# Kernel optimization log

Measured on AMD Instinct MI355X. Metric: run time of the kernel, lower is better.

## Reference

```python
import jax, jax.numpy as jnp
import numpy as np

N, E, D_EDGE, C, H, W, HID = 10000, 160000, 64, 16, 8, 8, 128


def setup_inputs() -> dict:
    key = jax.random.key(0)
    ks = jax.random.split(key, 7)
    x = jax.random.normal(ks[0], (N, C, H, W), jnp.float32)
    edge_attr = jax.random.normal(ks[1], (E, D_EDGE), jnp.float32)
    edge_index = jax.random.randint(ks[2], (2, E), 0, N, dtype=jnp.int64)
    W1 = jax.random.normal(ks[3], (D_EDGE, HID), jnp.float32) * 0.1
    b1 = jnp.zeros((HID,), jnp.float32)
    W2 = jax.random.normal(ks[4], (HID, 1), jnp.float32) * 0.1
    b2 = jnp.zeros((1,), jnp.float32)
    Wn = jax.random.normal(ks[5], (C, 3 * C), jnp.float32) * 0.1
    bn = jnp.zeros((C,), jnp.float32)
    return dict(x=x, edge_attr=edge_attr, W1=W1, b1=b1, W2=W2, b2=b2,
                Wn=Wn, bn=bn, edge_index=edge_index)


def _masked_scatter_softmax(logits, seg, mask, n):
    # softmax over edges grouped by seg, restricted to mask==True edges.
    # Masked edges get -inf logits -> exp 0 -> zero weight (same math as
    # boolean-indexing the edge subset in the torch original).
    neg = jnp.where(mask[:, None], logits, -jnp.inf)          # [E, 1]
    m = jax.ops.segment_max(neg, seg, num_segments=n)         # [N, 1]
    m = jnp.where(jnp.isfinite(m), m, 0.0)                    # empty segments
    e = jnp.exp(neg - m[seg])                                 # [E, 1], 0 where masked
    s = jax.ops.segment_sum(e, seg, num_segments=n)           # [N, 1]
    return e / jnp.maximum(s[seg], 1e-30)


def _flow(x, logits, row, col, mask, n):
    w = _masked_scatter_softmax(logits, row, mask, n)         # [E, 1]
    msg = x[col] * w[:, :, None, None]                        # [E, C, H, W]
    return jax.ops.segment_sum(msg, row, num_segments=n)      # [N, C, H, W]


def reference(x, edge_attr, W1, b1, W2, b2, Wn, bn, edge_index):
    row, col = edge_index[0], edge_index[1]
    # cls_net: MLP edge classifier producing per-edge logit [E, 1]
    h = jax.nn.relu(edge_attr @ W1 + b1)
    dec_edge_feats = h @ W2 + b2
    n = x.shape[0]
    flow_out = _flow(x, dec_edge_feats, row, col, row < col, n)
    flow_in = _flow(x, dec_edge_feats, row, col, row > col, n)
    flow = jnp.concatenate([x, flow_in, flow_out], axis=1)    # [N, 3C, H, W]
    # node_model: 1x1 conv over channels
    out = jnp.einsum('nchw,oc->nohw', flow, Wn) + bn[None, :, None, None]
    return out, dec_edge_feats
```

## Files before the change

### kernel.cpp

```cpp
#include <hip/hip_runtime.h>

#define N_NODES 10000
#define N_EDGES 160000
#define D_EDGE  64
#define C_CH    16
#define HW      64
#define HID     128
#define NODE_ELEMS 1024
#define NSEG    (2 * N_NODES)
#define CAP     64
#define MLPB    (N_EDGES / 64)
#define QUANTB  2500

typedef __attribute__((ext_vector_type(8))) short short8;
typedef __attribute__((ext_vector_type(4))) float f32x4;

__device__ __forceinline__ unsigned bf16_rne(float f) {
    unsigned u = __float_as_uint(f);
    return (u + 0x7FFFu + ((u >> 16) & 1u)) >> 16;
}
__device__ __forceinline__ short8 pack_bf16x8(float4 lo, float4 hi) {
    union { unsigned u[4]; short8 s; } r;
    r.u[0] = bf16_rne(lo.x) | (bf16_rne(lo.y) << 16);
    r.u[1] = bf16_rne(lo.z) | (bf16_rne(lo.w) << 16);
    r.u[2] = bf16_rne(hi.x) | (bf16_rne(hi.y) << 16);
    r.u[3] = bf16_rne(hi.z) | (bf16_rne(hi.w) << 16);
    return r.s;
}

__global__ __launch_bounds__(256) void k_prep(
    const float* __restrict__ W1, unsigned short* __restrict__ W1bfT,
    unsigned* __restrict__ zbase)
{
    if (blockIdx.x < 4) {
        int q  = blockIdx.x * 256 + threadIdx.x;
        int n  = q >> 3;
        int ko = (q & 7) * 8;
        #pragma unroll
        for (int i = 0; i < 8; ++i) {
            int k = ko + i;
            W1bfT[n * 64 + k] = (unsigned short)bf16_rne(W1[k * HID + n]);
        }
    } else {
        int idx = (blockIdx.x - 4) * 256 + threadIdx.x;
        for (int i = idx; i < NSEG; i += 64 * 256) zbase[i] = 0u;
    }
}

__device__ __forceinline__ unsigned pb4(float4 f, float inv) {
    int a = (int)rintf(f.x * inv) + 128;
    int b = (int)rintf(f.y * inv) + 128;
    int c = (int)rintf(f.z * inv) + 128;
    int d = (int)rintf(f.w * inv) + 128;
    a = min(255, max(0, a)); b = min(255, max(0, b));
    c = min(255, max(0, c)); d = min(255, max(0, d));
    return (unsigned)a | ((unsigned)b << 8) | ((unsigned)c << 16) | ((unsigned)d << 24);
}
__global__ __launch_bounds__(256) void k_mlpcast(
    const float* __restrict__ ea, const unsigned short* __restrict__ W1bfT,
    const float* __restrict__ b1, const float* __restrict__ W2,
    const float* __restrict__ b2,
    const int* __restrict__ row, const int* __restrict__ col,
    const float* __restrict__ x, unsigned char* __restrict__ xq,
    float* __restrict__ scale,
    float* __restrict__ dec,
    int* __restrict__ cursor, int2* __restrict__ bucket)
{
    const int tid = threadIdx.x;

    if (blockIdx.x >= MLPB) {
        const int wv = tid >> 6, ln = tid & 63;
        const int n  = (blockIdx.x - MLPB) * 4 + wv;
        const float4* xs = (const float4*)(x + (size_t)n * NODE_ELEMS) + ln * 4;
        float4 v0 = xs[0], v1 = xs[1], v2 = xs[2], v3 = xs[3];
        float m = fmaxf(fmaxf(fmaxf(fabsf(v0.x), fabsf(v0.y)),
                              fmaxf(fabsf(v0.z), fabsf(v0.w))),
                 fmaxf(fmaxf(fmaxf(fabsf(v1.x), fabsf(v1.y)),
                              fmaxf(fabsf(v1.z), fabsf(v1.w))),
                 fmaxf(fmaxf(fmaxf(fabsf(v2.x), fabsf(v2.y)),
                              fmaxf(fabsf(v2.z), fabsf(v2.w))),
                       fmaxf(fmaxf(fabsf(v3.x), fabsf(v3.y)),
                              fmaxf(fabsf(v3.z), fabsf(v3.w))))));
        #pragma unroll
        for (int off = 1; off < 64; off <<= 1)
            m = fmaxf(m, __shfl_xor(m, off));
        m = fmaxf(m, 1e-20f);
        float inv = 127.0f / m;
        uint4 o;
        o.x = pb4(v0, inv); o.y = pb4(v1, inv);
        o.z = pb4(v2, inv); o.w = pb4(v3, inv);
        ((uint4*)(xq + (size_t)n * NODE_ELEMS))[ln] = o;
        if (ln == 0) scale[n] = m * (1.0f / 127.0f);
        return;
    }

    __shared__ float s_w2[HID], s_b1[HID];
    __shared__ float s_logit[64];

    const int eb = blockIdx.x * 64;
    if (tid < HID) { s_w2[tid] = W2[tid]; s_b1[tid] = b1[tid]; }

    const int lane = tid & 63, w = tid >> 6;
    const int i15 = lane & 15, g = lane >> 4;
    const int m = w * 16 + i15;

    short8 bfrag[2][8];
    #pragma unroll
    for (int kt = 0; kt < 2; ++kt)
        #pragma unroll
        for (int t = 0; t < 8; ++t)
            bfrag[kt][t] = *(const short8*)&W1bfT[(t * 16 + i15) * 64 + kt * 32 + g * 8];

    short8 afrag[2];
    #pragma unroll
    for (int kt = 0; kt < 2; ++kt) {
        const float4* src = (const float4*)&ea[(size_t)(eb + m) * D_EDGE + kt * 32 + g * 8];
        afrag[kt] = pack_bf16x8(src[0], src[1]);
    }

    f32x4 acc[8];
    #pragma unroll
    for (int t = 0; t < 8; ++t) acc[t] = (f32x4){0.f, 0.f, 0.f, 0.f};
    #pragma unroll
    for (int kt = 0; kt < 2; ++kt)
        #pragma unroll
        for (int t = 0; t < 8; ++t)
            acc[t] = __builtin_amdgcn_mfma_f32_16x16x32_bf16(afrag[kt], bfrag[kt][t],
                                                             acc[t], 0, 0, 0);
    __syncthreads();

    float loc[4] = {0.f, 0.f, 0.f, 0.f};
    #pragma unroll
    for (int t = 0; t < 8; ++t) {
        float w2v = s_w2[t * 16 + i15];
        float bv  = s_b1[t * 16 + i15];
        #pragma unroll
        for (int r = 0; r < 4; ++r)
            loc[r] = fmaf(fmaxf(acc[t][r] + bv, 0.f), w2v, loc[r]);
    }
    #pragma unroll
    for (int r = 0; r < 4; ++r) {
        #pragma unroll
        for (int off = 1; off < 16; off <<= 1)
            loc[r] += __shfl_xor(loc[r], off);
    }
    if (i15 == 0) {
        #pragma unroll
        for (int r = 0; r < 4; ++r)
            s_logit[w * 16 + g * 4 + r] = loc[r];
    }
    __syncthreads();

    if (tid < 64) {
        int e = eb + tid;
        float logit = s_logit[tid] + b2[0];
        dec[e] = logit;
        int r = row[e], c = col[e];
        if (r != c) {
            float ex = expf(logit);
            int seg = 2 * r + ((r < c) ? 0 : 1);
            int pos = atomicAdd(&cursor[seg], 1);
            if (pos < CAP)
                bucket[((size_t)seg << 6) + pos] = make_int2(c, __float_as_int(ex));
        }
    }
}

__device__ __forceinline__ void acc8(float* A, uint2 v, float ws) {
    A[0] = fmaf(ws, (float)( v.x        & 255u), A[0]);
    A[1] = fmaf(ws, (float)((v.x >>  8) & 255u), A[1]);
    A[2] = fmaf(ws, (float)((v.x >> 16) & 255u), A[2]);
    A[3] = fmaf(ws, (float)( v.x >> 24        ), A[3]);
    A[4] = fmaf(ws, (float)( v.y        & 255u), A[4]);
    A[5] = fmaf(ws, (float)((v.y >>  8) & 255u), A[5]);
    A[6] = fmaf(ws, (float)((v.y >> 16) & 255u), A[6]);
    A[7] = fmaf(ws, (float)( v.y >> 24        ), A[7]);
}

__global__ __launch_bounds__(128) void k_gather(
    const float* __restrict__ x, const unsigned char* __restrict__ xq,
    const float* __restrict__ scale,
    const int* __restrict__ cursor, const int2* __restrict__ bucket,
    const float* __restrict__ Wn, const float* __restrict__ bn,
    float* __restrict__ out)
{
    const int n = blockIdx.x;
    const int t = threadIdx.x;

    __shared__ float sflow[2][NODE_ELEMS];
    __shared__ float sW[C_CH * 3 * C_CH];
    __shared__ float sbn[C_CH];
    __shared__ int2  s_ecw[2 * CAP];
    __shared__ float s_ex[2 * CAP];

    #pragma unroll
    for (int i = 0; i < 6; ++i) sW[i * 128 + t] = Wn[i * 128 + t];
    if (t < C_CH) sbn[t] = bn[t];

    const int c0  = min(cursor[2 * n],     CAP);
    const int c1  = min(cursor[2 * n + 1], CAP);
    const int tot = c0 + c1;
    if (t < tot) {
        int2 e = (t < c0) ? bucket[((size_t)(2 * n) << 6) + t]
                          : bucket[((size_t)(2 * n + 1) << 6) + t - c0];
        float ex = __int_as_float(e.y);
        s_ex[t] = ex;
        e.y = __float_as_int(ex * scale[e.x]);
        s_ecw[t] = e;
    }
    __syncthreads();

    float sum0 = 0.f, sum1 = 0.f;
    for (int i = 0; i < c0; ++i)   sum0 += s_ex[i];
    for (int i = c0; i < tot; ++i) sum1 += s_ex[i];

    float a[8] = {0,0,0,0,0,0,0,0};
    float b[8] = {0,0,0,0,0,0,0,0};
    float wsA = 0.f, wsB = 0.f;
    const uint2* xqt = (const uint2*)xq + t;

#define FMAJ(J) { float ws = __int_as_float(s_ecw[i + (J)].y);                \
                  if (i + (J) < c0) { acc8(a, v[J], ws); wsA += ws; }         \
                  else              { acc8(b, v[J], ws); wsB += ws; } }

    int i = 0;
    for (; i + 16 <= tot; i += 16) {
        uint2 v[16];
        #pragma unroll
        for (int j = 0; j < 16; ++j) v[j] = xqt[(size_t)s_ecw[i + j].x * 128];
        #pragma unroll
        for (int j = 0; j < 16; ++j) FMAJ(j)
    }
    for (; i + 8 <= tot; i += 8) {
        uint2 v[8];
        #pragma unroll
        for (int j = 0; j < 8; ++j) v[j] = xqt[(size_t)s_ecw[i + j].x * 128];
        #pragma unroll
        for (int j = 0; j < 8; ++j) FMAJ(j)
    }
    for (; i + 4 <= tot; i += 4) {
        uint2 v[4];
        #pragma unroll
        for (int j = 0; j < 4; ++j) v[j] = xqt[(size_t)s_ecw[i + j].x * 128];
        #pragma unroll
        for (int j = 0; j < 4; ++j) FMAJ(j)
    }
    for (; i < tot; ++i) {
        uint2 v[1];
        v[0] = xqt[(size_t)s_ecw[i].x * 128];
        FMAJ(0)
    }
#undef FMAJ

    const float r0 = 1.0f / fmaxf(sum0, 1e-30f);
    const float r1 = 1.0f / fmaxf(sum1, 1e-30f);
    const float o0 = 128.0f * wsA, o1 = 128.0f * wsB;
    float4 f;
    f.x = (a[0]-o0)*r0; f.y = (a[1]-o0)*r0; f.z = (a[2]-o0)*r0; f.w = (a[3]-o0)*r0;
    ((float4*)sflow[0])[t * 2] = f;
    f.x = (a[4]-o0)*r0; f.y = (a[5]-o0)*r0; f.z = (a[6]-o0)*r0; f.w = (a[7]-o0)*r0;
    ((float4*)sflow[0])[t * 2 + 1] = f;
    f.x = (b[0]-o1)*r1; f.y = (b[1]-o1)*r1; f.z = (b[2]-o1)*r1; f.w = (b[3]-o1)*r1;
    ((float4*)sflow[1])[t * 2] = f;
    f.x = (b[4]-o1)*r1; f.y = (b[5]-o1)*r1; f.z = (b[6]-o1)*r1; f.w = (b[7]-o1)*r1;
    ((float4*)sflow[1])[t * 2 + 1] = f;
    __syncthreads();

    const int hw = t & 63;
    const int ob = t >> 6;
    const float* xb0 = x + (size_t)n * NODE_ELEMS + hw;
    float vx[C_CH], vi[C_CH], vo[C_CH];
    #pragma unroll
    for (int c = 0; c < C_CH; ++c) {
        vx[c] = xb0[c * HW];
        vo[c] = sflow[0][c * HW + hw];
        vi[c] = sflow[1][c * HW + hw];
    }
    float* outb = out + (size_t)n * NODE_ELEMS;
    #pragma unroll
    for (int k = 0; k < 8; ++k) {
        int o = ob * 8 + k;
        float acc = sbn[o];
        const float* wr = &sW[o * 3 * C_CH];
        #pragma unroll
        for (int c = 0; c < C_CH; ++c) {
            acc = fmaf(vx[c], wr[c],            acc);
            acc = fmaf(vi[c], wr[C_CH + c],     acc);
            acc = fmaf(vo[c], wr[2 * C_CH + c], acc);
        }
        outb[o * HW + hw] = acc;
    }
}

extern "C" void kernel_launch(void* const* d_in, const int* in_sizes, int n_in,
                              void* d_out, int out_size, void* d_ws, size_t ws_size,
                              hipStream_t stream)
{
    const float* x         = (const float*)d_in[0];
    const float* edge_attr = (const float*)d_in[1];
    const float* W1        = (const float*)d_in[2];
    const float* b1        = (const float*)d_in[3];
    const float* W2        = (const float*)d_in[4];
    const float* b2        = (const float*)d_in[5];
    const float* Wn        = (const float*)d_in[6];
    const float* bn        = (const float*)d_in[7];
    const int*   eidx      = (const int*)d_in[8];
    const int*   row       = eidx;
    const int*   col       = eidx + N_EDGES;

    float* out = (float*)d_out;
    float* dec = out + (size_t)N_NODES * NODE_ELEMS;

    unsigned char* xq     = (unsigned char*)d_ws;
    float*         scale  = (float*)(xq + (size_t)N_NODES * NODE_ELEMS);
    int2*          bucket = (int2*)(scale + N_NODES);
    int*           cursor = (int*)(bucket + (size_t)NSEG * CAP);
    unsigned short* W1bfT = (unsigned short*)(cursor + NSEG);

    k_prep<<<68, 256, 0, stream>>>(W1, W1bfT, (unsigned*)cursor);
    k_mlpcast<<<MLPB + QUANTB, 256, 0, stream>>>(edge_attr, W1bfT, b1, W2, b2,
                                                 row, col, x, xq, scale,
                                                 dec, cursor, bucket);
    k_gather<<<N_NODES, 128, 0, stream>>>(x, xq, scale, cursor,
                                          bucket, Wn, bn, out);
}
```

Baseline: 86.31 us.

## Use bf16 MFMA for node 1x1 conv and hoist bucket atomics early

The per-node 1x1 channel conv in the gather kernel is rewritten as a bf16 MFMA 16x16x32 GEMM. x and both flows are staged transposed in padded bf16 shared memory, and Wn is pre-transposed and converted to bf16 in the prep kernel. In the MLP kernel, the row/col loads and bucket-slot atomics are moved before the MFMA work so their latency overlaps with compute. This cuts FP32 FMA work and shared-memory traffic but adds bf16 rounding error to the output.

```diff
diff --git a/kernel.cpp b/kernel.cpp
--- a/kernel.cpp
+++ b/kernel.cpp
@@ -11,6 +11,7 @@
 #define CAP     64
 #define MLPB    (N_EDGES / 64)
 #define QUANTB  2500
+#define XPITCH  72
 
 typedef __attribute__((ext_vector_type(8))) short short8;
 typedef __attribute__((ext_vector_type(4))) float f32x4;
@@ -29,11 +30,13 @@
 }
 
 __global__ __launch_bounds__(256) void k_prep(
-    const float* __restrict__ W1, unsigned short* __restrict__ W1bfT,
+    const float* __restrict__ W1, const float* __restrict__ Wn,
+    unsigned short* __restrict__ W1bfT, unsigned short* __restrict__ WnTb,
     unsigned* __restrict__ zbase)
 {
+    int tid = threadIdx.x;
     if (blockIdx.x < 4) {
-        int q  = blockIdx.x * 256 + threadIdx.x;
+        int q  = blockIdx.x * 256 + tid;
         int n  = q >> 3;
         int ko = (q & 7) * 8;
         #pragma unroll
@@ -41,8 +44,17 @@
             int k = ko + i;
             W1bfT[n * 64 + k] = (unsigned short)bf16_rne(W1[k * HID + n]);
         }
+    } else if (blockIdx.x == 4) {
+        int q = tid * 4;
+        int o = q >> 6, k0 = q & 63;
+        #pragma unroll
+        for (int i = 0; i < 4; ++i) {
+            int k = k0 + i;
+            WnTb[o * 64 + k] =
+                (k < 48) ? (unsigned short)bf16_rne(Wn[o * 48 + k]) : 0;
+        }
     } else {
-        int idx = (blockIdx.x - 4) * 256 + threadIdx.x;
+        int idx = (blockIdx.x - 5) * 256 + tid;
         for (int i = idx; i < NSEG; i += 64 * 256) zbase[i] = 0u;
     }
 }
@@ -98,6 +110,17 @@
     __shared__ float s_logit[64];
 
     const int eb = blockIdx.x * 64;
+
+    int e_c = 0, pos = -1, seg = 0;
+    if (tid < 64) {
+        int e = eb + tid;
+        int r = row[e]; e_c = col[e];
+        if (r != e_c) {
+            seg = 2 * r + ((r < e_c) ? 0 : 1);
+            pos = atomicAdd(&cursor[seg], 1);
+        }
+    }
+
     if (tid < HID) { s_w2[tid] = W2[tid]; s_b1[tid] = b1[tid]; }
 
     const int lane = tid & 63, w = tid >> 6;
@@ -152,16 +175,11 @@
     __syncthreads();
 
     if (tid < 64) {
-        int e = eb + tid;
         float logit = s_logit[tid] + b2[0];
-        dec[e] = logit;
-        int r = row[e], c = col[e];
-        if (r != c) {
+        dec[eb + tid] = logit;
+        if (pos >= 0 && pos < CAP) {
             float ex = expf(logit);
-            int seg = 2 * r + ((r < c) ? 0 : 1);
-            int pos = atomicAdd(&cursor[seg], 1);
-            if (pos < CAP)
-                bucket[((size_t)seg << 6) + pos] = make_int2(c, __float_as_int(ex));
+            bucket[((size_t)seg << 6) + pos] = make_int2(e_c, __float_as_int(ex));
         }
     }
 }
@@ -181,21 +199,20 @@
     const float* __restrict__ x, const unsigned char* __restrict__ xq,
     const float* __restrict__ scale,
     const int* __restrict__ cursor, const int2* __restrict__ bucket,
-    const float* __restrict__ Wn, const float* __restrict__ bn,
+    const unsigned short* __restrict__ WnTb, const float* __restrict__ bn,
     float* __restrict__ out)
 {
     const int n = blockIdx.x;
     const int t = threadIdx.x;
 
-    __shared__ float sflow[2][NODE_ELEMS];
-    __shared__ float sW[C_CH * 3 * C_CH];
-    __shared__ float sbn[C_CH];
+    __shared__ __align__(16) unsigned short sxf[64 * XPITCH];
     __shared__ int2  s_ecw[2 * CAP];
     __shared__ float s_ex[2 * CAP];
 
-    #pragma unroll
-    for (int i = 0; i < 6; ++i) sW[i * 128 + t] = Wn[i * 128 + t];
-    if (t < C_CH) sbn[t] = bn[t];
+    {
+        int zr = t >> 1, zk = 48 + (t & 1) * 8;
+        *(uint4*)&sxf[zr * XPITCH + zk] = make_uint4(0, 0, 0, 0);
+    }
 
     const int c0  = min(cursor[2 * n],     CAP);
     const int c1  = min(cursor[2 * n + 1], CAP);
@@ -252,43 +269,42 @@
     }
 #undef FMAJ
 
+    const int c_of_t = t >> 3, hw0 = (t & 7) * 8;
+    const float4* xsrc = (const float4*)(x + (size_t)n * NODE_ELEMS) + t * 2;
+    float4 xv0 = xsrc[0], xv1 = xsrc[1];
+
     const float r0 = 1.0f / fmaxf(sum0, 1e-30f);
     const float r1 = 1.0f / fmaxf(sum1, 1e-30f);
     const float o0 = 128.0f * wsA, o1 = 128.0f * wsB;
-    float4 f;
-    f.x = (a[0]-o0)*r0; f.y = (a[1]-o0)*r0; f.z = (a[2]-o0)*r0; f.w = (a[3]-o0)*r0;
-    ((float4*)sflow[0])[t * 2] = f;
-    f.x = (a[4]-o0)*r0; f.y = (a[5]-o0)*r0; f.z = (a[6]-o0)*r0; f.w = (a[7]-o0)*r0;
-    ((float4*)sflow[0])[t * 2 + 1] = f;
-    f.x = (b[0]-o1)*r1; f.y = (b[1]-o1)*r1; f.z = (b[2]-o1)*r1; f.w = (b[3]-o1)*r1;
-    ((float4*)sflow[1])[t * 2] = f;
-    f.x = (b[4]-o1)*r1; f.y = (b[5]-o1)*r1; f.z = (b[6]-o1)*r1; f.w = (b[7]-o1)*r1;
-    ((float4*)sflow[1])[t * 2 + 1] = f;
+    float xv[8] = {xv0.x, xv0.y, xv0.z, xv0.w, xv1.x, xv1.y, xv1.z, xv1.w};
+    #pragma unroll
+    for (int j = 0; j < 8; ++j) {
+        unsigned short* rowp = &sxf[(hw0 + j) * XPITCH];
+        rowp[     c_of_t] = (unsigned short)bf16_rne(xv[j]);
+        rowp[16 + c_of_t] = (unsigned short)bf16_rne((b[j] - o1) * r1);
+        rowp[32 + c_of_t] = (unsigned short)bf16_rne((a[j] - o0) * r0);
+    }
     __syncthreads();
 
-    const int hw = t & 63;
-    const int ob = t >> 6;
-    const float* xb0 = x + (size_t)n * NODE_ELEMS + hw;
-    float vx[C_CH], vi[C_CH], vo[C_CH];
-    #pragma unroll
-    for (int c = 0; c < C_CH; ++c) {
-        vx[c] = xb0[c * HW];
-        vo[c] = sflow[0][c * HW + hw];
-        vi[c] = sflow[1][c * HW + hw];
-    }
+    const int lane = t & 63, wv = t >> 6;
+    const int i15 = lane & 15, g = lane >> 4;
+    const float bno = bn[i15];
     float* outb = out + (size_t)n * NODE_ELEMS;
-    #pragma unroll
-    for (int k = 0; k < 8; ++k) {
-        int o = ob * 8 + k;
-        float acc = sbn[o];
-        const float* wr = &sW[o * 3 * C_CH];
-        #pragma unroll
-        for (int c = 0; c < C_CH; ++c) {
-            acc = fmaf(vx[c], wr[c],            acc);
-            acc = fmaf(vi[c], wr[C_CH + c],     acc);
-            acc = fmaf(vo[c], wr[2 * C_CH + c], acc);
-        }
-        outb[o * HW + hw] = acc;
+
+    #pragma unroll
+    for (int mt = 0; mt < 2; ++mt) {
+        const int mrow = (wv * 2 + mt) * 16;
+        f32x4 accm = (f32x4){bno, bno, bno, bno};
+        #pragma unroll
+        for (int kt = 0; kt < 2; ++kt) {
+            short8 af = *(const short8*)&sxf[(mrow + i15) * XPITCH + kt * 32 + g * 8];
+            short8 bf = *(const short8*)&WnTb[i15 * 64 + kt * 32 + g * 8];
+            accm = __builtin_amdgcn_mfma_f32_16x16x32_bf16(af, bf, accm, 0, 0, 0);
+        }
+        const int hwb = mrow + g * 4;
+        #pragma unroll
+        for (int r = 0; r < 4; ++r)
+            outb[i15 * 64 + hwb + r] = accm[r];
     }
 }
 
@@ -316,11 +332,12 @@
     int2*          bucket = (int2*)(scale + N_NODES);
     int*           cursor = (int*)(bucket + (size_t)NSEG * CAP);
     unsigned short* W1bfT = (unsigned short*)(cursor + NSEG);
-
-    k_prep<<<68, 256, 0, stream>>>(W1, W1bfT, (unsigned*)cursor);
+    unsigned short* WnTb  = W1bfT + D_EDGE * HID;
+
+    k_prep<<<69, 256, 0, stream>>>(W1, Wn, W1bfT, WnTb, (unsigned*)cursor);
     k_mlpcast<<<MLPB + QUANTB, 256, 0, stream>>>(edge_attr, W1bfT, b1, W2, b2,
                                                  row, col, x, xq, scale,
                                                  dec, cursor, bucket);
     k_gather<<<N_NODES, 128, 0, stream>>>(x, xq, scale, cursor,
-                                          bucket, Wn, bn, out);
-}
+                                          bucket, WnTb, bn, out);
+}
```

Measured after the change: 80.89 us. 6.3% less time.
